# Performance work log

Hardware: AMD Instinct MI355X
Metric: run time of the kernel (lower is better)

Reference implementation:

```python
import jax, jax.numpy as jnp
import numpy as np

H, W = 72, 128            # raster_h, raster_w
THICK = 0.03              # raster_thickness
SHARP = 80.0              # sigmoid sharpness
RESAMPLE_N = 96           # resample count used for geometric matching costs
PTS_W, TAN_W, CURV_W, OVL_W = 5.0, 1.0, 0.5, 2.0


def _safe_norm(x, axis=-1):
    # faithful to torch.norm; tiny floor only to keep sqrt grad finite
    return jnp.sqrt(jnp.maximum((x * x).sum(axis), 1e-12))


def _grid_xy(h, w):
    ys = jnp.linspace(0.0, 1.0, h)
    xs = jnp.linspace(0.0, 1.0, w)
    yy, xx = jnp.meshgrid(ys, xs, indexing='ij')
    return jnp.stack([xx, yy], axis=-1).reshape(-1, 2)  # [H*W, 2]


def _prepare_mask(vis):
    # mirrors _batched_prepare_curves: fallback to all-ones when <2 visible pts
    raw = vis > 0.5
    fallback = raw.sum(-1) < 2
    return jnp.where(fallback[:, None], 1.0, raw.astype(vis.dtype))  # [m,p]


def _soft_mask(points, point_mask, grid):
    # points [m,p,2], grid [HW,2] -> sigmoid distance field [m, HW]
    seg_a = points[:, :-1]
    ab = points[:, 1:] - seg_a                              # [m,S,2]
    denom = jnp.maximum((ab * ab).sum(-1), 1e-8)            # [m,S]
    seg_valid = (point_mask[:, :-1] * point_mask[:, 1:]) > 0.5
    pts = grid[None, :, None, :]                            # [1,HW,1,2]
    ap = pts - seg_a[:, None]                               # [m,HW,S,2]
    t = jnp.clip((ap * ab[:, None]).sum(-1) / denom[:, None], 0.0, 1.0)
    proj = seg_a[:, None] + t[..., None] * ab[:, None]      # [m,HW,S,2]
    dist = _safe_norm(pts - proj)                           # [m,HW,S]
    dist = jnp.where(seg_valid[:, None, :], dist, jnp.inf)
    min_dist = dist.min(-1)                                 # [m,HW]
    # fallback: curves with no valid segment use nearest visible point
    pdist = _safe_norm(grid[None, :, None, :] - points[:, None])  # [m,HW,p]
    pdist = jnp.where(point_mask[:, None, :] > 0.5, pdist, jnp.inf)
    no_seg = ~seg_valid.any(-1)
    min_dist = jnp.where(no_seg[:, None], pdist.min(-1), min_dist)
    return jax.nn.sigmoid((THICK - min_dist) * SHARP)       # [m,HW]


def _resample(points, point_mask, num):
    # arclength resampling, mirrors _batched_resample_polyline
    m, p, _ = points.shape
    seg_valid = point_mask[:, :-1] * point_mask[:, 1:]
    seg_len = _safe_norm(points[:, 1:] - points[:, :-1]) * seg_valid  # [m,p-1]
    cum = jnp.concatenate([jnp.zeros((m, 1), points.dtype),
                           jnp.cumsum(seg_len, -1)], axis=-1)          # [m,p]
    total = cum[:, -1]
    base_t = jnp.linspace(0.0, 1.0, num)
    t = base_t[None, :] * total[:, None]                               # [m,num]
    idx = jax.vmap(lambda c, tt: jnp.searchsorted(c, tt, side='right'))(cum, t) - 1
    idx = jnp.clip(idx, 0, p - 2)
    left = jnp.take_along_axis(points[:, :-1], idx[..., None], axis=1)
    right = jnp.take_along_axis(points[:, 1:], idx[..., None], axis=1)
    lt = jnp.take_along_axis(cum[:, :-1], idx, axis=1)
    rt = jnp.take_along_axis(cum[:, 1:], idx, axis=1)
    alpha = ((t - lt) / jnp.maximum(rt - lt, 1e-8))[..., None]
    out = left + alpha * (right - left)
    return jnp.where((total < 1e-8)[:, None, None], points[:, :1, :], out)


def _pt2poly(A, B):
    # A [qa,r,2] sample points; B [qb,r,2] polylines -> mean min dist [qa,qb]
    seg_a = B[:, :-1]
    ab = B[:, 1:] - seg_a                                   # [qb,S,2]
    denom = jnp.maximum((ab * ab).sum(-1), 1e-8)            # [qb,S]
    pts = A[:, None, :, None, :]                            # [qa,1,r,1,2]
    ap = pts - seg_a[None, :, None]                         # [qa,qb,r,S,2]
    t = jnp.clip((ap * ab[None, :, None]).sum(-1) / denom[None, :, None], 0.0, 1.0)
    proj = seg_a[None, :, None] + t[..., None] * ab[None, :, None]
    dist = _safe_norm(pts - proj)                           # [qa,qb,r,S]
    return dist.min(-1).mean(-1)                            # [qa,qb]


def _tangents(pts):
    # central differences, endpoints one-sided, unit-normalized
    fwd = jnp.concatenate([pts[:, 1:2] - pts[:, 0:1],
                           pts[:, 2:] - pts[:, :-2],
                           pts[:, -1:] - pts[:, -2:-1]], axis=1)
    n = jnp.maximum(jnp.sqrt((fwd * fwd).sum(-1, keepdims=True)), 1e-8)
    return fwd / n


def _smooth_l1(x):
    a = jnp.abs(x)
    return jnp.where(a < 1.0, 0.5 * a * a, a - 0.5)


def lane_match_cost(pred_pts, gt_pts, gt_vis):
    grid = _grid_xy(H, W)
    m_pred = jnp.ones(pred_pts.shape[:2], pred_pts.dtype)
    m_gt = _prepare_mask(gt_vis)
    # geometric pairwise costs on resampled curves
    pred_rs = _resample(pred_pts, m_pred, RESAMPLE_N)       # [Q,r,2]
    gt_rs = _resample(gt_pts, m_gt, RESAMPLE_N)             # [G,r,2]
    sym = 0.5 * (_pt2poly(pred_rs, gt_rs) + _pt2poly(gt_rs, pred_rs).T)
    pt = _tangents(pred_rs)
    gt_t = _tangents(gt_rs)
    tan = 1.0 - jnp.abs((pt[:, None] * gt_t[None]).sum(-1)).mean(-1)
    ps = pred_rs[:, 2:] - 2 * pred_rs[:, 1:-1] + pred_rs[:, :-2]
    gs = gt_rs[:, 2:] - 2 * gt_rs[:, 1:-1] + gt_rs[:, :-2]
    curv = _smooth_l1(ps[:, None] - gs[None]).mean((-1, -2))
    # soft raster overlap (1 - soft IoU)
    pm = _soft_mask(pred_pts, m_pred, grid)                 # [Q,HW]
    gm = _soft_mask(gt_pts, m_gt, grid)                     # [G,HW]
    inter = pm @ gm.T
    union = pm.sum(-1)[:, None] + gm.sum(-1)[None, :] - inter
    overlap = 1.0 - inter / jnp.maximum(union, 1e-8)
    return PTS_W * sym + TAN_W * tan + CURV_W * curv + OVL_W * overlap


def setup_inputs() -> dict:
    key = jax.random.key(0)
    k1, k2, k3 = jax.random.split(key, 3)
    Q, G, P = 100, 50, 24
    pred_pts = jax.random.uniform(k1, (Q, P, 2), dtype=jnp.float32)
    gt_pts = jax.random.uniform(k2, (G, P, 2), dtype=jnp.float32)
    gt_vis = jax.random.uniform(k3, (G, P), dtype=jnp.float32)
    return {"pred_pts": pred_pts, "gt_pts": gt_pts, "gt_vis": gt_vis}


def reference(pred_pts, gt_pts, gt_vis):
    return lane_match_cost(pred_pts, gt_pts, gt_vis)  # [Q,G] match cost
```

## Files before the change

### kernel.cpp

```cpp
#include <hip/hip_runtime.h>
#include <hip/hip_bf16.h>
#include <math.h>

#define Q_N 100
#define G_N 50
#define P_N 24
#define RS_N 96
#define GRID_N 9216
#define THICK 0.03f
#define SHARP 80.0f
#define PTS_W 5.0f
#define TAN_W 1.0f
#define CURV_W 0.5f
#define OVL_W 2.0f

#define PRS_OFF  0
#define GRS_OFF  19200
#define PMB_OFF  28800
#define GMB_OFF  489600
#define ROWP_OFF 720000
#define ROWG_OFF 720900

typedef float    f32x2 __attribute__((ext_vector_type(2)));
typedef _Float16 h16x2 __attribute__((ext_vector_type(2)));

__device__ __forceinline__ float smooth_l1(float x) {
    float a = fabsf(x);
    return (a < 1.0f) ? 0.5f * a * a : a - 0.5f;
}

#if __has_builtin(__builtin_amdgcn_fdot2)
__device__ __forceinline__ float fdot2(unsigned a, unsigned b, float c) {
    return __builtin_amdgcn_fdot2(__builtin_bit_cast(h16x2, a),
                                  __builtin_bit_cast(h16x2, b), c, false);
}
#else
__device__ __forceinline__ float fdot2(unsigned a, unsigned b, float c) {
    h16x2 ha = __builtin_bit_cast(h16x2, a);
    h16x2 hb = __builtin_bit_cast(h16x2, b);
    return c + (float)ha.x * (float)hb.x + (float)ha.y * (float)hb.y;
}
#endif

__global__ __launch_bounds__(256)
void mask_kernel(const float* __restrict__ pred,
                 const float* __restrict__ gt,
                 const float* __restrict__ vis,
                 float* __restrict__ ws) {
    int row   = blockIdx.x / 9;
    int chunk = blockIdx.x % 9;
    int tid = threadIdx.x;
    bool isPred = row < Q_N;
    __shared__ float ptx[P_N], pty[P_N], pvv[P_N];
    __shared__ float4 seg[P_N-1];
    __shared__ float  sinv[P_N-1];
    __shared__ int s_noseg;
    __shared__ float wsum[4];
    __shared__ float cum[P_N];
    __shared__ float s_total;

    if (tid < P_N) {
        const float* src = isPred ? pred + row * (P_N*2) : gt + (row - Q_N) * (P_N*2);
        float2 p = ((const float2*)src)[tid];
        ptx[tid] = p.x; pty[tid] = p.y;
    }
    if (tid == 0) {
        s_noseg = 1;
        if (isPred) {
            for (int k = 0; k < P_N; k++) pvv[k] = 1.0f;
        } else {
            const float* v = vis + (row - Q_N) * P_N;
            int cnt = 0;
            for (int k = 0; k < P_N; k++) {
                int r = (v[k] > 0.5f) ? 1 : 0;
                cnt += r;
                pvv[k] = (float)r;
            }
            if (cnt < 2) for (int k = 0; k < P_N; k++) pvv[k] = 1.0f;
        }
    }
    __syncthreads();
    if (tid < P_N-1) {
        bool v = pvv[tid] * pvv[tid+1] > 0.5f;
        if (v) {
            float ax = ptx[tid], ay = pty[tid];
            float abx = ptx[tid+1]-ax, aby = pty[tid+1]-ay;
            seg[tid] = make_float4(ax, ay, abx, aby);
            sinv[tid] = 1.0f / fmaxf(abx*abx + aby*aby, 1e-8f);
            s_noseg = 0;
        } else {
            seg[tid] = make_float4(1e18f, 1e18f, 0.0f, 0.0f);
            sinv[tid] = 0.0f;
        }
    }
    __syncthreads();

    int g0 = chunk * 1024 + tid * 4;
    float xs[4], ys[4], m2[4];
    #pragma unroll
    for (int u = 0; u < 4; u++) {
        int g = g0 + u;
        xs[u] = (float)(g & 127) * (1.0f/127.0f);
        ys[u] = (float)(g >> 7)  * (1.0f/71.0f);
        m2[u] = 3.0e38f;
    }
    for (int k = 0; k < P_N-1; k++) {
        float4 sg = seg[k];
        float inv = sinv[k];
        #pragma unroll
        for (int u = 0; u < 4; u++) {
            float apx = xs[u] - sg.x, apy = ys[u] - sg.y;
            float t = (apx*sg.z + apy*sg.w) * inv;
            t = fminf(fmaxf(t, 0.0f), 1.0f);
            float dx = apx - t*sg.z, dy = apy - t*sg.w;
            m2[u] = fminf(m2[u], dx*dx + dy*dy);
        }
    }
    if (s_noseg) {
        #pragma unroll
        for (int u = 0; u < 4; u++) m2[u] = 3.0e38f;
        for (int k = 0; k < P_N; k++) {
            if (pvv[k] > 0.5f) {
                #pragma unroll
                for (int u = 0; u < 4; u++) {
                    float dx = xs[u] - ptx[k], dy = ys[u] - pty[k];
                    m2[u] = fminf(m2[u], dx*dx + dy*dy);
                }
            }
        }
    }
    ushort4 o;
    unsigned short* ov = &o.x;
    float lsum = 0.0f;
    #pragma unroll
    for (int u = 0; u < 4; u++) {
        float mind = sqrtf(fmaxf(m2[u], 1e-12f));
        float z = (THICK - mind) * SHARP;
        float s = 1.0f / (1.0f + __expf(-z));
        _Float16 h = (_Float16)s;
        ov[u] = __builtin_bit_cast(unsigned short, h);
        lsum += (float)h;
    }
    unsigned short* base = (unsigned short*)(ws + (isPred ? PMB_OFF : GMB_OFF))
                         + (size_t)(isPred ? row : row - Q_N) * GRID_N;
    ((ushort4*)base)[g0 >> 2] = o;

    #pragma unroll
    for (int off = 32; off > 0; off >>= 1) lsum += __shfl_down(lsum, off);
    if ((tid & 63) == 0) wsum[tid >> 6] = lsum;
    __syncthreads();
    if (tid == 0) {
        float s = (wsum[0] + wsum[1]) + (wsum[2] + wsum[3]);
        if (isPred) ws[ROWP_OFF + row*9 + chunk] = s;
        else        ws[ROWG_OFF + (row - Q_N)*9 + chunk] = s;
    }

    if (chunk == 0) {
        if (tid == 0) {
            float c = 0.0f;
            cum[0] = 0.0f;
            for (int k = 0; k < P_N-1; k++) {
                float dx = ptx[k+1]-ptx[k], dy = pty[k+1]-pty[k];
                float len = sqrtf(fmaxf(dx*dx + dy*dy, 1e-12f));
                float valid = pvv[k]*pvv[k+1];
                c += len * valid;
                cum[k+1] = c;
            }
            s_total = c;
        }
        __syncthreads();
        float total = s_total;
        if (tid < RS_N) {
            float ox, oy;
            if (total < 1e-8f) {
                ox = ptx[0]; oy = pty[0];
            } else {
                float t = ((float)tid / 95.0f) * total;
                int idx = -1;
                for (int k = 0; k < P_N; k++) idx += (cum[k] <= t) ? 1 : 0;
                idx = min(max(idx, 0), P_N-2);
                float lt = cum[idx], rt = cum[idx+1];
                float alpha = (t - lt) / fmaxf(rt - lt, 1e-8f);
                ox = ptx[idx] + alpha * (ptx[idx+1]-ptx[idx]);
                oy = pty[idx] + alpha * (pty[idx+1]-pty[idx]);
            }
            float* dst = isPred ? ws + PRS_OFF + row * (RS_N*2)
                                : ws + GRS_OFF + (row - Q_N) * (RS_N*2);
            dst[2*tid]   = ox;
            dst[2*tid+1] = oy;
        }
    }
}

__global__ __launch_bounds__(256)
void pair_kernel(const float* __restrict__ ws, float* __restrict__ out) {
    int bi = blockIdx.x / 25;
    int bj = blockIdx.x % 25;
    int i0 = bi*2, j0 = bj*2;
    int tid = threadIdx.x;
    int w = tid >> 6;
    int l = tid & 63;
    int wi = w >> 1, wj = w & 1;
    int i = i0 + wi, j = j0 + wj;

    __shared__ float Apts[2][RS_N*2], Bpts[2][RS_N*2];
    __shared__ float4 Aseg[2][RS_N-1], Bseg[2][RS_N-1];
    __shared__ float  AInv[2][RS_N-1], BInv[2][RS_N-1];

    float e_rp = 0.0f, e_rg = 0.0f;
    if (l < 9) {
        e_rp = ws[ROWP_OFF + i*9 + l];
        e_rg = ws[ROWG_OFF + j*9 + l];
    }

    if (tid < 192) {
        int side = tid / 96;
        int r = (tid / 48) & 1;
        int o = tid % 48;
        const float4* src = (const float4*)(ws + (side ? GRS_OFF + (j0+r)*(RS_N*2)
                                                       : PRS_OFF + (i0+r)*(RS_N*2)));
        ((float4*)(side ? Bpts[r] : Apts[r]))[o] = src[o];
    }
    __syncthreads();
    for (int q = tid; q < 4*(RS_N-1); q += 256) {
        int side = q / (2*(RS_N-1));
        int rr = (q / (RS_N-1)) & 1;
        int s = q % (RS_N-1);
        const float* P = side ? Bpts[rr] : Apts[rr];
        float ax = P[2*s], ay = P[2*s+1];
        float abx = P[2*s+2]-ax, aby = P[2*s+3]-ay;
        float inv = 1.0f / fmaxf(abx*abx + aby*aby, 1e-8f);
        if (side) { Bseg[rr][s] = make_float4(ax,ay,abx,aby); BInv[rr][s] = inv; }
        else      { Aseg[rr][s] = make_float4(ax,ay,abx,aby); AInv[rr][s] = inv; }
    }
    __syncthreads();

    const uint4* pa = (const uint4*)((const unsigned short*)(ws + PMB_OFF) + (size_t)i * GRID_N);
    const uint4* pb = (const uint4*)((const unsigned short*)(ws + GMB_OFF) + (size_t)j * GRID_N);
    float dot = 0.0f;
    #pragma unroll 6
    for (int c = 0; c < 18; c++) {
        uint4 a = pa[c*64 + l];
        uint4 b = pb[c*64 + l];
        dot = fdot2(a.x, b.x, dot);
        dot = fdot2(a.y, b.y, dot);
        dot = fdot2(a.z, b.z, dot);
        dot = fdot2(a.w, b.w, dot);
    }

    bool bSide = l >= 32;
    int h = l & 31;
    const float*  myP = bSide ? Bpts[wj] : Apts[wi];
    const float4* SG  = bSide ? Aseg[wi] : Bseg[wj];
    const float*  SI  = bSide ? AInv[wi] : BInv[wj];
    f32x2 px01 = { myP[6*h+0], myP[6*h+2] };
    f32x2 py01 = { myP[6*h+1], myP[6*h+3] };
    float px2 = myP[6*h+4], py2 = myP[6*h+5];
    float m20 = 3.0e38f, m21 = 3.0e38f, m22 = 3.0e38f;
    for (int s = 0; s < RS_N-1; s++) {
        float4 sg = SG[s];
        float inv = SI[s];
        {
            f32x2 apx = px01 - sg.x;
            f32x2 apy = py01 - sg.y;
            f32x2 dt = apx*sg.z + apy*sg.w;
            f32x2 t = dt * inv;
            t.x = fminf(fmaxf(t.x, 0.0f), 1.0f);
            t.y = fminf(fmaxf(t.y, 0.0f), 1.0f);
            f32x2 dx = apx - t*sg.z;
            f32x2 dy = apy - t*sg.w;
            f32x2 d2 = dx*dx + dy*dy;
            m20 = fminf(m20, d2.x);
            m21 = fminf(m21, d2.y);
        }
        {
            float apx = px2-sg.x, apy = py2-sg.y;
            float t = fminf(fmaxf((apx*sg.z + apy*sg.w)*inv, 0.0f), 1.0f);
            float dx = apx - t*sg.z, dy = apy - t*sg.w;
            m22 = fminf(m22, dx*dx + dy*dy);
        }
    }
    float cham = sqrtf(fmaxf(m20, 1e-12f)) + sqrtf(fmaxf(m21, 1e-12f))
               + sqrtf(fmaxf(m22, 1e-12f));

    const float* AX = Apts[wi];
    const float* BX = Bpts[wj];
    float tsum = 0.0f, csum = 0.0f;
    #pragma unroll
    for (int rep = 0; rep < 2; rep++) {
        int p = l + rep*64;
        if (p < RS_N) {
            int pl = (p == 0) ? 0 : p-1;
            int pr = (p == RS_N-1) ? RS_N-1 : p+1;
            float tax = AX[2*pr]-AX[2*pl], tay = AX[2*pr+1]-AX[2*pl+1];
            float na = fmaxf(sqrtf(tax*tax + tay*tay), 1e-8f);
            float tbx = BX[2*pr]-BX[2*pl], tby = BX[2*pr+1]-BX[2*pl+1];
            float nb = fmaxf(sqrtf(tbx*tbx + tby*tby), 1e-8f);
            tsum += fabsf((tax*tbx + tay*tby) / (na*nb));
            if (p < RS_N-2) {
                float psx = AX[2*p+4] - 2.0f*AX[2*p+2] + AX[2*p];
                float psy = AX[2*p+5] - 2.0f*AX[2*p+3] + AX[2*p+1];
                float gsx = BX[2*p+4] - 2.0f*BX[2*p+2] + BX[2*p];
                float gsy = BX[2*p+5] - 2.0f*BX[2*p+3] + BX[2*p+1];
                csum += smooth_l1(psx - gsx) + smooth_l1(psy - gsy);
            }
        }
    }

    #pragma unroll
    for (int off = 32; off > 0; off >>= 1) {
        cham += __shfl_down(cham, off);
        tsum += __shfl_down(tsum, off);
        csum += __shfl_down(csum, off);
        dot  += __shfl_down(dot,  off);
    }
    #pragma unroll
    for (int off = 8; off > 0; off >>= 1) {
        e_rp += __shfl_down(e_rp, off);
        e_rg += __shfl_down(e_rg, off);
    }

    if (l == 0) {
        float sym  = cham * (1.0f/192.0f);
        float tanv = 1.0f - tsum * (1.0f/96.0f);
        float cuv  = csum * (1.0f/188.0f);
        float uni  = e_rp + e_rg - dot;
        float ovl  = 1.0f - dot / fmaxf(uni, 1e-8f);
        out[i * G_N + j] = PTS_W * sym + TAN_W * tanv + CURV_W * cuv + OVL_W * ovl;
    }
}

extern "C" void kernel_launch(void* const* d_in, const int* in_sizes, int n_in,
                              void* d_out, int out_size, void* d_ws, size_t ws_size,
                              hipStream_t stream) {
    (void)in_sizes; (void)n_in; (void)out_size; (void)ws_size;
    const float* pred = (const float*)d_in[0];
    const float* gt   = (const float*)d_in[1];
    const float* vis  = (const float*)d_in[2];
    float* out = (float*)d_out;
    float* ws  = (float*)d_ws;

    mask_kernel<<<(Q_N + G_N) * 9, 256, 0, stream>>>(pred, gt, vis, ws);
    pair_kernel<<<50 * 25, 256, 0, stream>>>(ws, out);
}
```

Before: 55.58 us.

## Compute mask intersections with MFMA split-K GEMM kernel and use fast math intrinsics

Moves the soft-mask intersection dot products out of pair_kernel into a new inter_kernel. That kernel runs a padded 112x64 fp16 GEMM on MFMA 16x16x32 instructions, splits K into 9 chunks, and writes partial sums that pair_kernel reduces. This removes the per-pair re-reading of two 18KB fp16 rows from cache in every pair block, at the cost of an extra kernel launch and a workspace layout change. It also uses packed f32x2 math for the mask distance loop and swaps in hardware rcp/sqrt intrinsics, which slightly reduce precision.

```diff
diff --git a/kernel.cpp b/kernel.cpp
--- a/kernel.cpp
+++ b/kernel.cpp
@@ -17,30 +17,33 @@
 #define PRS_OFF  0
 #define GRS_OFF  19200
 #define PMB_OFF  28800
-#define GMB_OFF  489600
-#define ROWP_OFF 720000
-#define ROWG_OFF 720900
+#define GMB_OFF  544896
+#define ROWP_OFF 839808
+#define ROWG_OFF 840708
+#define INTP_OFF 841216
 
 typedef float    f32x2 __attribute__((ext_vector_type(2)));
-typedef _Float16 h16x2 __attribute__((ext_vector_type(2)));
+typedef float    f32x4 __attribute__((ext_vector_type(4)));
+typedef _Float16 f16x8 __attribute__((ext_vector_type(8)));
 
 __device__ __forceinline__ float smooth_l1(float x) {
     float a = fabsf(x);
     return (a < 1.0f) ? 0.5f * a * a : a - 0.5f;
 }
-
-#if __has_builtin(__builtin_amdgcn_fdot2)
-__device__ __forceinline__ float fdot2(unsigned a, unsigned b, float c) {
-    return __builtin_amdgcn_fdot2(__builtin_bit_cast(h16x2, a),
-                                  __builtin_bit_cast(h16x2, b), c, false);
-}
+__device__ __forceinline__ float fast_rcp(float x) {
+#if __has_builtin(__builtin_amdgcn_rcpf)
+    return __builtin_amdgcn_rcpf(x);
 #else
-__device__ __forceinline__ float fdot2(unsigned a, unsigned b, float c) {
-    h16x2 ha = __builtin_bit_cast(h16x2, a);
-    h16x2 hb = __builtin_bit_cast(h16x2, b);
-    return c + (float)ha.x * (float)hb.x + (float)ha.y * (float)hb.y;
-}
+    return 1.0f / x;
 #endif
+}
+__device__ __forceinline__ float fast_sqrt(float x) {
+#if __has_builtin(__builtin_amdgcn_sqrtf)
+    return __builtin_amdgcn_sqrtf(x);
+#else
+    return sqrtf(x);
+#endif
+}
 
 __global__ __launch_bounds__(256)
 void mask_kernel(const float* __restrict__ pred,
@@ -86,7 +89,7 @@
             float ax = ptx[tid], ay = pty[tid];
             float abx = ptx[tid+1]-ax, aby = pty[tid+1]-ay;
             seg[tid] = make_float4(ax, ay, abx, aby);
-            sinv[tid] = 1.0f / fmaxf(abx*abx + aby*aby, 1e-8f);
+            sinv[tid] = fast_rcp(fmaxf(abx*abx + aby*aby, 1e-8f));
             s_noseg = 0;
         } else {
             seg[tid] = make_float4(1e18f, 1e18f, 0.0f, 0.0f);
@@ -96,34 +99,44 @@
     __syncthreads();
 
     int g0 = chunk * 1024 + tid * 4;
-    float xs[4], ys[4], m2[4];
-    #pragma unroll
-    for (int u = 0; u < 4; u++) {
-        int g = g0 + u;
-        xs[u] = (float)(g & 127) * (1.0f/127.0f);
-        ys[u] = (float)(g >> 7)  * (1.0f/71.0f);
-        m2[u] = 3.0e38f;
-    }
+    float y  = (float)(g0 >> 7) * (1.0f/71.0f);
+    float x0 = (float)(g0 & 127) * (1.0f/127.0f);
+    f32x2 xs01 = { x0,                  x0 + 1.0f/127.0f };
+    f32x2 xs23 = { x0 + 2.0f/127.0f,    x0 + 3.0f/127.0f };
+    f32x2 m01 = {3.0e38f, 3.0e38f}, m23 = {3.0e38f, 3.0e38f};
+    #pragma unroll
     for (int k = 0; k < P_N-1; k++) {
         float4 sg = seg[k];
         float inv = sinv[k];
-        #pragma unroll
-        for (int u = 0; u < 4; u++) {
-            float apx = xs[u] - sg.x, apy = ys[u] - sg.y;
-            float t = (apx*sg.z + apy*sg.w) * inv;
-            t = fminf(fmaxf(t, 0.0f), 1.0f);
-            float dx = apx - t*sg.z, dy = apy - t*sg.w;
-            m2[u] = fminf(m2[u], dx*dx + dy*dy);
-        }
-    }
+        float apy = y - sg.y;
+        float dwy = apy * sg.w;
+        f32x2 apx01 = xs01 - sg.x;
+        f32x2 apx23 = xs23 - sg.x;
+        f32x2 t01 = (apx01*sg.z + dwy) * inv;
+        f32x2 t23 = (apx23*sg.z + dwy) * inv;
+        t01.x = fminf(fmaxf(t01.x, 0.0f), 1.0f);
+        t01.y = fminf(fmaxf(t01.y, 0.0f), 1.0f);
+        t23.x = fminf(fmaxf(t23.x, 0.0f), 1.0f);
+        t23.y = fminf(fmaxf(t23.y, 0.0f), 1.0f);
+        f32x2 dx01 = apx01 - t01*sg.z;
+        f32x2 dy01 = apy   - t01*sg.w;
+        f32x2 dx23 = apx23 - t23*sg.z;
+        f32x2 dy23 = apy   - t23*sg.w;
+        f32x2 d01 = dx01*dx01 + dy01*dy01;
+        f32x2 d23 = dx23*dx23 + dy23*dy23;
+        m01.x = fminf(m01.x, d01.x); m01.y = fminf(m01.y, d01.y);
+        m23.x = fminf(m23.x, d23.x); m23.y = fminf(m23.y, d23.y);
+    }
+    float m2[4] = { m01.x, m01.y, m23.x, m23.y };
     if (s_noseg) {
+        float xs[4] = { xs01.x, xs01.y, xs23.x, xs23.y };
         #pragma unroll
         for (int u = 0; u < 4; u++) m2[u] = 3.0e38f;
         for (int k = 0; k < P_N; k++) {
             if (pvv[k] > 0.5f) {
                 #pragma unroll
                 for (int u = 0; u < 4; u++) {
-                    float dx = xs[u] - ptx[k], dy = ys[u] - pty[k];
+                    float dx = xs[u] - ptx[k], dy = y - pty[k];
                     m2[u] = fminf(m2[u], dx*dx + dy*dy);
                 }
             }
@@ -134,9 +147,9 @@
     float lsum = 0.0f;
     #pragma unroll
     for (int u = 0; u < 4; u++) {
-        float mind = sqrtf(fmaxf(m2[u], 1e-12f));
+        float mind = fast_sqrt(fmaxf(m2[u], 1e-12f));
         float z = (THICK - mind) * SHARP;
-        float s = 1.0f / (1.0f + __expf(-z));
+        float s = fast_rcp(1.0f + __expf(-z));
         _Float16 h = (_Float16)s;
         ov[u] = __builtin_bit_cast(unsigned short, h);
         lsum += (float)h;
@@ -192,6 +205,31 @@
     }
 }
 
+__global__ __launch_bounds__(64)
+void inter_kernel(float* __restrict__ ws) {
+    int bid = blockIdx.x;
+    int mt = bid % 7;
+    int nt = (bid / 7) & 3;
+    int kc = bid / 28;
+    int l = threadIdx.x;
+    const unsigned short* PMB = (const unsigned short*)(ws + PMB_OFF);
+    const unsigned short* GMB = (const unsigned short*)(ws + GMB_OFF);
+    int i0 = mt*16, j0 = nt*16, k0 = kc*1024;
+    const f16x8* pa = (const f16x8*)(PMB + (size_t)(i0 + (l & 15)) * GRID_N + k0 + 8*(l >> 4));
+    const f16x8* pb = (const f16x8*)(GMB + (size_t)(j0 + (l & 15)) * GRID_N + k0 + 8*(l >> 4));
+    f32x4 acc = {0.0f, 0.0f, 0.0f, 0.0f};
+    #pragma unroll 8
+    for (int s = 0; s < 32; s++) {
+        acc = __builtin_amdgcn_mfma_f32_16x16x32_f16(pa[s*4], pb[s*4], acc, 0, 0, 0);
+    }
+    float* dst = ws + INTP_OFF + kc * 7168;
+    int r0 = 4*(l >> 4), c = l & 15;
+    #pragma unroll
+    for (int v = 0; v < 4; v++) {
+        dst[(i0 + r0 + v) * 64 + (j0 + c)] = acc[v];
+    }
+}
+
 __global__ __launch_bounds__(256)
 void pair_kernel(const float* __restrict__ ws, float* __restrict__ out) {
     int bi = blockIdx.x / 25;
@@ -207,8 +245,9 @@
     __shared__ float4 Aseg[2][RS_N-1], Bseg[2][RS_N-1];
     __shared__ float  AInv[2][RS_N-1], BInv[2][RS_N-1];
 
-    float e_rp = 0.0f, e_rg = 0.0f;
+    float e_ip = 0.0f, e_rp = 0.0f, e_rg = 0.0f;
     if (l < 9) {
+        e_ip = ws[INTP_OFF + l*7168 + i*64 + j];
         e_rp = ws[ROWP_OFF + i*9 + l];
         e_rg = ws[ROWG_OFF + j*9 + l];
     }
@@ -229,24 +268,11 @@
         const float* P = side ? Bpts[rr] : Apts[rr];
         float ax = P[2*s], ay = P[2*s+1];
         float abx = P[2*s+2]-ax, aby = P[2*s+3]-ay;
-        float inv = 1.0f / fmaxf(abx*abx + aby*aby, 1e-8f);
+        float inv = fast_rcp(fmaxf(abx*abx + aby*aby, 1e-8f));
         if (side) { Bseg[rr][s] = make_float4(ax,ay,abx,aby); BInv[rr][s] = inv; }
         else      { Aseg[rr][s] = make_float4(ax,ay,abx,aby); AInv[rr][s] = inv; }
     }
     __syncthreads();
-
-    const uint4* pa = (const uint4*)((const unsigned short*)(ws + PMB_OFF) + (size_t)i * GRID_N);
-    const uint4* pb = (const uint4*)((const unsigned short*)(ws + GMB_OFF) + (size_t)j * GRID_N);
-    float dot = 0.0f;
-    #pragma unroll 6
-    for (int c = 0; c < 18; c++) {
-        uint4 a = pa[c*64 + l];
-        uint4 b = pb[c*64 + l];
-        dot = fdot2(a.x, b.x, dot);
-        dot = fdot2(a.y, b.y, dot);
-        dot = fdot2(a.z, b.z, dot);
-        dot = fdot2(a.w, b.w, dot);
-    }
 
     bool bSide = l >= 32;
     int h = l & 31;
@@ -256,22 +282,23 @@
     f32x2 px01 = { myP[6*h+0], myP[6*h+2] };
     f32x2 py01 = { myP[6*h+1], myP[6*h+3] };
     float px2 = myP[6*h+4], py2 = myP[6*h+5];
-    float m20 = 3.0e38f, m21 = 3.0e38f, m22 = 3.0e38f;
+    f32x2 m01 = {3.0e38f, 3.0e38f};
+    float m22 = 3.0e38f;
+    #pragma unroll 5
     for (int s = 0; s < RS_N-1; s++) {
         float4 sg = SG[s];
         float inv = SI[s];
         {
             f32x2 apx = px01 - sg.x;
             f32x2 apy = py01 - sg.y;
-            f32x2 dt = apx*sg.z + apy*sg.w;
-            f32x2 t = dt * inv;
+            f32x2 t = (apx*sg.z + apy*sg.w) * inv;
             t.x = fminf(fmaxf(t.x, 0.0f), 1.0f);
             t.y = fminf(fmaxf(t.y, 0.0f), 1.0f);
             f32x2 dx = apx - t*sg.z;
             f32x2 dy = apy - t*sg.w;
             f32x2 d2 = dx*dx + dy*dy;
-            m20 = fminf(m20, d2.x);
-            m21 = fminf(m21, d2.y);
+            m01.x = fminf(m01.x, d2.x);
+            m01.y = fminf(m01.y, d2.y);
         }
         {
             float apx = px2-sg.x, apy = py2-sg.y;
@@ -280,8 +307,8 @@
             m22 = fminf(m22, dx*dx + dy*dy);
         }
     }
-    float cham = sqrtf(fmaxf(m20, 1e-12f)) + sqrtf(fmaxf(m21, 1e-12f))
-               + sqrtf(fmaxf(m22, 1e-12f));
+    float cham = fast_sqrt(fmaxf(m01.x, 1e-12f)) + fast_sqrt(fmaxf(m01.y, 1e-12f))
+               + fast_sqrt(fmaxf(m22, 1e-12f));
 
     const float* AX = Apts[wi];
     const float* BX = Bpts[wj];
@@ -293,10 +320,10 @@
             int pl = (p == 0) ? 0 : p-1;
             int pr = (p == RS_N-1) ? RS_N-1 : p+1;
             float tax = AX[2*pr]-AX[2*pl], tay = AX[2*pr+1]-AX[2*pl+1];
-            float na = fmaxf(sqrtf(tax*tax + tay*tay), 1e-8f);
+            float na = fmaxf(fast_sqrt(tax*tax + tay*tay), 1e-8f);
             float tbx = BX[2*pr]-BX[2*pl], tby = BX[2*pr+1]-BX[2*pl+1];
-            float nb = fmaxf(sqrtf(tbx*tbx + tby*tby), 1e-8f);
-            tsum += fabsf((tax*tbx + tay*tby) / (na*nb));
+            float nb = fmaxf(fast_sqrt(tbx*tbx + tby*tby), 1e-8f);
+            tsum += fabsf((tax*tbx + tay*tby) * fast_rcp(na*nb));
             if (p < RS_N-2) {
                 float psx = AX[2*p+4] - 2.0f*AX[2*p+2] + AX[2*p];
                 float psy = AX[2*p+5] - 2.0f*AX[2*p+3] + AX[2*p+1];
@@ -312,10 +339,10 @@
         cham += __shfl_down(cham, off);
         tsum += __shfl_down(tsum, off);
         csum += __shfl_down(csum, off);
-        dot  += __shfl_down(dot,  off);
     }
     #pragma unroll
     for (int off = 8; off > 0; off >>= 1) {
+        e_ip += __shfl_down(e_ip, off);
         e_rp += __shfl_down(e_rp, off);
         e_rg += __shfl_down(e_rg, off);
     }
@@ -324,8 +351,8 @@
         float sym  = cham * (1.0f/192.0f);
         float tanv = 1.0f - tsum * (1.0f/96.0f);
         float cuv  = csum * (1.0f/188.0f);
-        float uni  = e_rp + e_rg - dot;
-        float ovl  = 1.0f - dot / fmaxf(uni, 1e-8f);
+        float uni  = e_rp + e_rg - e_ip;
+        float ovl  = 1.0f - e_ip / fmaxf(uni, 1e-8f);
         out[i * G_N + j] = PTS_W * sym + TAN_W * tanv + CURV_W * cuv + OVL_W * ovl;
     }
 }
@@ -341,5 +368,6 @@
     float* ws  = (float*)d_ws;
 
     mask_kernel<<<(Q_N + G_N) * 9, 256, 0, stream>>>(pred, gt, vis, ws);
+    inter_kernel<<<7 * 4 * 9, 64, 0, stream>>>(ws);
     pair_kernel<<<50 * 25, 256, 0, stream>>>(ws, out);
 }
```

Measured after the change: 46.53 us. 16.3% less time.
